# Kernel optimization log

Measured on AMD Instinct MI355X. Metric: run time of the kernel, lower is better.

## Reference

```python
import jax, jax.numpy as jnp
import numpy as np

EPS = 1e-5


def setup_inputs() -> dict:
    key = jax.random.key(0)
    ks = jax.random.split(key, 5)
    N, E, D, L = 10000, 160000, 512, 3
    x = jax.random.normal(ks[0], (N, D), dtype=jnp.float32)
    src = jax.random.randint(ks[1], (E,), 0, N, dtype=jnp.int64)
    dst = jax.random.randint(ks[2], (E,), 0, N, dtype=jnp.int64)
    gamma = jnp.ones((L, D), dtype=jnp.float32)
    beta = jnp.zeros((L, D), dtype=jnp.float32)
    # glorot-ish scale so ReLU stack stays well-conditioned
    W = jax.random.normal(ks[3], (L, D, D), dtype=jnp.float32) * (1.0 / np.sqrt(D))
    b = jnp.zeros((L, D), dtype=jnp.float32)
    return {"x": x, "src": src, "dst": dst, "gamma": gamma, "beta": beta, "W": W, "b": b}


def reference(x, src, dst, gamma, beta, W, b):
    N = x.shape[0]
    ones = jnp.ones(src.shape[0], dtype=x.dtype)
    # DGL GraphConv norm='both': src side uses out-degree, dst side uses in-degree
    out_deg = jnp.clip(jax.ops.segment_sum(ones, src, num_segments=N), 1.0)
    in_deg = jnp.clip(jax.ops.segment_sum(ones, dst, num_segments=N), 1.0)
    src_norm = (out_deg ** -0.5)[:, None]  # [N,1]
    dst_norm = (in_deg ** -0.5)[:, None]   # [N,1]
    n_layers = gamma.shape[0]
    for i in range(n_layers):
        # BatchNorm1d (training mode: batch mean, biased variance)
        mu = jnp.mean(x, axis=0)
        var = jnp.var(x, axis=0)
        x = (x - mu) * jax.lax.rsqrt(var + EPS) * gamma[i] + beta[i]
        h = x * src_norm
        agg = jax.ops.segment_sum(h[src], dst, num_segments=N) * dst_norm
        x = jax.nn.relu(agg @ W[i] + b[i])
    return x
```

## Files before the change

### kernel.cpp

```cpp
#include <hip/hip_runtime.h>
#include <hip/hip_bf16.h>

constexpr int N = 10000;
constexpr int D = 512;
constexpr int E = 160000;
constexpr int L = 3;
constexpr float EPS = 1e-5f;

constexpr int NSHARD = 8;
constexpr int SHCOL = D / NSHARD;

typedef _Float16 half8 __attribute__((ext_vector_type(8)));
typedef _Float16 half2v __attribute__((ext_vector_type(2)));
typedef float floatx4 __attribute__((ext_vector_type(4)));

__device__ __forceinline__ void glds16(const _Float16* g, _Float16* l) {
    __builtin_amdgcn_global_load_lds(
        (const __attribute__((address_space(1))) uint32_t*)(g),
        (__attribute__((address_space(3))) uint32_t*)(l),
        16, 0, 0);
}

constexpr int DEG_BLOCKS  = (E + 255) / 256;
constexpr int CONV_BLOCKS = 100;
constexpr int TW_BLOCKS   = L * 256;
constexpr int MEGA_BLOCKS = DEG_BLOCKS + CONV_BLOCKS + TW_BLOCKS;

__global__ __launch_bounds__(256) void mega_setup(
    const int* __restrict__ src, const int* __restrict__ dst,
    const float* __restrict__ x, const float* __restrict__ W,
    int* __restrict__ out_deg, int* __restrict__ in_deg,
    _Float16* __restrict__ x16, float* __restrict__ stats0,
    _Float16* __restrict__ Wt) {
    __shared__ float tb[32][33];
    int bid = blockIdx.x;
    int tid = threadIdx.x;
    if (bid < DEG_BLOCKS) {
        int e = bid * 256 + tid;
        if (e < E) {
            atomicAdd(&out_deg[src[e]], 1);
            atomicAdd(&in_deg[dst[e]], 1);
        }
    } else if (bid < DEG_BLOCKS + CONV_BLOCKS) {
        int b = bid - DEG_BLOCKS;
        int r0 = b * 100;
        int r1 = r0 + 100; if (r1 > N) r1 = N;
        int c2 = tid * 2;
        float s0 = 0.f, s1 = 0.f, q0 = 0.f, q1 = 0.f;
        for (int r = r0; r < r1; ++r) {
            float2 v = *(const float2*)(x + (size_t)r * D + c2);
            s0 += v.x; q0 += v.x * v.x;
            s1 += v.y; q1 += v.y * v.y;
            half2v h; h[0] = (_Float16)v.x; h[1] = (_Float16)v.y;
            *(half2v*)(x16 + (size_t)r * D + c2) = h;
        }
        atomicAdd(&stats0[c2], s0);
        atomicAdd(&stats0[c2 + 1], s1);
        atomicAdd(&stats0[D + c2], q0);
        atomicAdd(&stats0[D + c2 + 1], q1);
    } else {
        int b = bid - DEG_BLOCKS - CONV_BLOCKS;
        int l = b >> 8;
        int t = b & 255;
        int k0 = (t >> 4) * 32, n0 = (t & 15) * 32;
        int tx = tid & 31, ty = tid >> 5;
        const float* Wl = W + (size_t)l * D * D;
        _Float16* Wtl = Wt + (size_t)l * D * D;
        for (int i = 0; i < 32; i += 8)
            tb[ty + i][tx] = Wl[(size_t)(k0 + ty + i) * D + n0 + tx];
        __syncthreads();
        for (int i = 0; i < 32; i += 8)
            Wtl[(size_t)(n0 + ty + i) * D + k0 + tx] = (_Float16)tb[tx][ty + i];
    }
}

__global__ void scan_indeg(const int* __restrict__ in_deg,
                           const int* __restrict__ out_deg,
                           int* __restrict__ off, int* __restrict__ cursor,
                           float* __restrict__ src_norm, float* __restrict__ dst_norm) {
    __shared__ int lsum[1024];
    int t = threadIdx.x;
    const int chunk = (N + 1023) / 1024;
    int start = t * chunk;
    int end = start + chunk; if (end > N) end = N;
    int s = 0;
    for (int i = start; i < end; ++i) s += in_deg[i];
    lsum[t] = s;
    __syncthreads();
    for (int d = 1; d < 1024; d <<= 1) {
        int v = (t >= d) ? lsum[t - d] : 0;
        __syncthreads();
        lsum[t] += v;
        __syncthreads();
    }
    int excl = (t == 0) ? 0 : lsum[t - 1];
    for (int i = start; i < end; ++i) {
        off[i] = excl;
        cursor[i] = excl;
        excl += in_deg[i];
        int od = out_deg[i]; if (od < 1) od = 1;
        int id = in_deg[i];  if (id < 1) id = 1;
        src_norm[i] = rsqrtf((float)od);
        dst_norm[i] = rsqrtf((float)id);
    }
    if (t == 1023) off[N] = lsum[1023];
}

__global__ void csr_fill(const int* __restrict__ src, const int* __restrict__ dst,
                         int* __restrict__ cursor, int* __restrict__ csr_src) {
    int e = blockIdx.x * blockDim.x + threadIdx.x;
    if (e >= E) return;
    int d = dst[e];
    int pos = atomicAdd(&cursor[d], 1);
    csr_src[pos] = src[e];
}

__global__ __launch_bounds__(256) void aggregate_bn_shard(
    const _Float16* __restrict__ x, const int* __restrict__ off,
    const int* __restrict__ csr_src, const float* __restrict__ src_norm,
    const float* __restrict__ dst_norm, const float* __restrict__ stats,
    const float* __restrict__ gamma, const float* __restrict__ beta,
    _Float16* __restrict__ agg) {
    int shard = blockIdx.x & 7;
    int blk   = blockIdx.x >> 3;
    int wave  = threadIdx.x >> 6;
    int wid   = blk * 4 + wave;
    int lane  = threadIdx.x & 63;
    int half  = lane >> 5;
    int cl    = lane & 31;
    int c0    = shard * SHCOL + cl * 2;

    const float invN = 1.0f / (float)N;
    float2 sv = *(const float2*)(stats + c0);
    float2 qv = *(const float2*)(stats + D + c0);
    float2 gm = *(const float2*)(gamma + c0);
    float2 bt = *(const float2*)(beta + c0);
    float mu0 = sv.x * invN, mu1 = sv.y * invN;
    float var0 = qv.x * invN - mu0 * mu0;
    float var1 = qv.y * invN - mu1 * mu1;
    float sc0 = gm.x * rsqrtf(var0 + EPS);
    float sc1 = gm.y * rsqrtf(var1 + EPS);
    float sh0 = bt.x - mu0 * sc0;
    float sh1 = bt.y - mu1 * sc1;

    int e0 = off[wid], e1 = off[wid + 1];
    const _Float16* xs = x + c0;
    float a0 = 0.f, a1 = 0.f, b0 = 0.f, b1 = 0.f, tA = 0.f, tB = 0.f;
    int e = e0 + half;
    for (; e + 2 < e1; e += 4) {
        int sA = csr_src[e];
        int sB = csr_src[e + 2];
        float nA = src_norm[sA];
        float nB = src_norm[sB];
        half2v vA = *(const half2v*)(xs + (size_t)sA * D);
        half2v vB = *(const half2v*)(xs + (size_t)sB * D);
        a0 += (float)vA[0] * nA; a1 += (float)vA[1] * nA; tA += nA;
        b0 += (float)vB[0] * nB; b1 += (float)vB[1] * nB; tB += nB;
    }
    for (; e < e1; e += 2) {
        int sA = csr_src[e];
        float nA = src_norm[sA];
        half2v vA = *(const half2v*)(xs + (size_t)sA * D);
        a0 += (float)vA[0] * nA; a1 += (float)vA[1] * nA; tA += nA;
    }
    a0 += b0; a1 += b1;
    float t = tA + tB;
    a0 += __shfl_xor(a0, 32);
    a1 += __shfl_xor(a1, 32);
    t  += __shfl_xor(t, 32);
    if (half == 0) {
        float dn = dst_norm[wid];
        half2v o;
        o[0] = (_Float16)(dn * (sc0 * a0 + sh0 * t));
        o[1] = (_Float16)(dn * (sc1 * a1 + sh1 * t));
        *(half2v*)(agg + (size_t)wid * D + c0) = o;
    }
}

template <typename OutT, bool STATS>
__global__ __launch_bounds__(128) void mm_f16_relu(
    const _Float16* __restrict__ A, const _Float16* __restrict__ Bt,
    const float* __restrict__ bias, OutT* __restrict__ C, int M,
    float* __restrict__ stats) {
    __shared__ __align__(16) _Float16 As[2][64 * 64];
    __shared__ __align__(16) _Float16 Bs[2][128 * 64];
    const int tid  = threadIdx.x;
    const int wave = tid >> 6;
    const int lane = tid & 63;
    const int quad = lane >> 4;
    const int l16  = lane & 15;
    const int row0 = blockIdx.x * 64;
    const int col0 = blockIdx.y * 128;
    const int wn   = wave * 64;

    const int srl = lane >> 3;
    const int sq  = lane & 7;
    const int sqs = (sq ^ srl) * 8;

    const _Float16* gA[4];
    const _Float16* gB[8];
#pragma unroll
    for (int j = 0; j < 4; ++j) {
        int ar = row0 + wave * 32 + j * 8 + srl;
        if (ar >= M) ar = M - 1;
        gA[j] = A + (size_t)ar * D + sqs;
    }
#pragma unroll
    for (int j = 0; j < 8; ++j) {
        int br = col0 + wave * 64 + j * 8 + srl;
        gB[j] = Bt + (size_t)br * D + sqs;
    }

    const int l7 = l16 & 7;
    const int swz0 = (quad ^ l7) * 8;
    const int swz1 = ((4 + quad) ^ l7) * 8;

    floatx4 acc[4][4] = {};

    auto stage = [&](int buf, int k0) {
        _Float16* as = As[buf] + (wave * 32) * 64;
        _Float16* bs = Bs[buf] + (wave * 64) * 64;
#pragma unroll
        for (int j = 0; j < 4; ++j)
            glds16(gA[j] + k0, as + j * 8 * 64);
#pragma unroll
        for (int j = 0; j < 8; ++j)
            glds16(gB[j] + k0, bs + j * 8 * 64);
    };

    stage(0, 0);
    __syncthreads();

    int cur = 0;
    for (int kt = 0; kt < 8; ++kt) {
        if (kt < 7) stage(cur ^ 1, (kt + 1) * 64);
        const _Float16* asb = As[cur];
        const _Float16* bsb = Bs[cur];
        half8 af0[4], af1[4], bf0[4], bf1[4];
#pragma unroll
        for (int i = 0; i < 4; ++i) {
            int r = i * 16 + l16;
            af0[i] = *(const half8*)(asb + r * 64 + swz0);
            af1[i] = *(const half8*)(asb + r * 64 + swz1);
        }
#pragma unroll
        for (int j = 0; j < 4; ++j) {
            int r = wn + j * 16 + l16;
            bf0[j] = *(const half8*)(bsb + r * 64 + swz0);
            bf1[j] = *(const half8*)(bsb + r * 64 + swz1);
        }
#pragma unroll
        for (int i = 0; i < 4; ++i)
#pragma unroll
            for (int j = 0; j < 4; ++j)
                acc[i][j] = __builtin_amdgcn_mfma_f32_16x16x32_f16(
                    af0[i], bf0[j], acc[i][j], 0, 0, 0);
#pragma unroll
        for (int i = 0; i < 4; ++i)
#pragma unroll
            for (int j = 0; j < 4; ++j)
                acc[i][j] = __builtin_amdgcn_mfma_f32_16x16x32_f16(
                    af1[i], bf1[j], acc[i][j], 0, 0, 0);
        __syncthreads();
        cur ^= 1;
    }

    float s[4] = {}, q[4] = {};
#pragma unroll
    for (int i = 0; i < 4; ++i) {
#pragma unroll
        for (int r = 0; r < 4; ++r) {
            int row = row0 + i * 16 + quad * 4 + r;
            bool valid = row < M;
#pragma unroll
            for (int j = 0; j < 4; ++j) {
                int col = col0 + wn + j * 16 + l16;
                float v = acc[i][j][r] + bias[col];
                v = v > 0.f ? v : 0.f;
                if (valid) {
                    C[(size_t)row * D + col] = (OutT)v;
                    if (STATS) { s[j] += v; q[j] += v * v; }
                }
            }
        }
    }
    if (STATS) {
#pragma unroll
        for (int j = 0; j < 4; ++j) {
            float sv = s[j], qv = q[j];
            sv += __shfl_xor(sv, 16); sv += __shfl_xor(sv, 32);
            qv += __shfl_xor(qv, 16); qv += __shfl_xor(qv, 32);
            if (quad == 0) {
                int col = col0 + wn + j * 16 + l16;
                atomicAdd(&stats[col], sv);
                atomicAdd(&stats[D + col], qv);
            }
        }
    }
}

extern "C" void kernel_launch(void* const* d_in, const int* in_sizes, int n_in,
                              void* d_out, int out_size, void* d_ws, size_t ws_size,
                              hipStream_t stream) {
    const float* x_in  = (const float*)d_in[0];
    const int*   src   = (const int*)d_in[1];
    const int*   dst   = (const int*)d_in[2];
    const float* gamma = (const float*)d_in[3];
    const float* beta  = (const float*)d_in[4];
    const float* W     = (const float*)d_in[5];
    const float* b     = (const float*)d_in[6];
    float* out = (float*)d_out;

    char* p = (char*)d_ws;
    _Float16* x16 = (_Float16*)p;  p += (size_t)N * D * 2;
    _Float16* agg = (_Float16*)p;  p += (size_t)N * D * 2;
    _Float16* Wt  = (_Float16*)p;  p += (size_t)L * D * D * 2;
    float* src_norm = (float*)p;   p += (size_t)N * 4;
    float* dst_norm = (float*)p;   p += (size_t)N * 4;
    int* out_deg   = (int*)p;      p += (size_t)N * 4;
    int* in_deg    = (int*)p;      p += (size_t)N * 4;
    float* stats0  = (float*)p;    p += 2 * D * 4;
    float* stats1  = (float*)p;    p += 2 * D * 4;
    float* stats2  = (float*)p;    p += 2 * D * 4;
    int* csr_off   = (int*)p;      p += (size_t)(N + 1) * 4;
    int* cursor    = (int*)p;      p += (size_t)N * 4;
    int* csr_src   = (int*)p;      p += (size_t)E * 4;

    float* stats_in[3] = {stats0, stats1, stats2};

    hipMemsetAsync(out_deg, 0, (2 * (size_t)N + 6 * D) * sizeof(int), stream);
    mega_setup<<<MEGA_BLOCKS, 256, 0, stream>>>(src, dst, x_in, W,
                                                out_deg, in_deg, x16, stats0, Wt);
    scan_indeg<<<1, 1024, 0, stream>>>(in_deg, out_deg, csr_off, cursor,
                                       src_norm, dst_norm);
    csr_fill<<<DEG_BLOCKS, 256, 0, stream>>>(src, dst, cursor, csr_src);

    dim3 mm_grid((N + 63) / 64, D / 128);
    const int agg_blocks = NSHARD * ((N + 3) / 4);

    for (int l = 0; l < L; ++l) {
        const float* gl  = gamma + (size_t)l * D;
        const float* bl  = beta + (size_t)l * D;
        const _Float16* Wl = Wt + (size_t)l * D * D;
        const float* bil = b + (size_t)l * D;

        aggregate_bn_shard<<<agg_blocks, 256, 0, stream>>>(
            x16, csr_off, csr_src, src_norm, dst_norm, stats_in[l], gl, bl, agg);
        if (l == L - 1) {
            mm_f16_relu<float, false><<<mm_grid, 128, 0, stream>>>(
                agg, Wl, bil, out, N, nullptr);
        } else {
            mm_f16_relu<_Float16, true><<<mm_grid, 128, 0, stream>>>(
                agg, Wl, bil, x16, N, stats_in[l + 1]);
        }
    }
}
```

Baseline: 346.0 us.

## Replace column-sharded aggregation with one wave per node using 16-byte loads

```diff
diff --git a/kernel.cpp b/kernel.cpp
--- a/kernel.cpp
+++ b/kernel.cpp
@@ -7,9 +7,6 @@
 constexpr int L = 3;
 constexpr float EPS = 1e-5f;
 
-constexpr int NSHARD = 8;
-constexpr int SHCOL = D / NSHARD;
-
 typedef _Float16 half8 __attribute__((ext_vector_type(8)));
 typedef _Float16 half2v __attribute__((ext_vector_type(2)));
 typedef float floatx4 __attribute__((ext_vector_type(4)));
@@ -22,7 +19,7 @@
 }
 
 constexpr int DEG_BLOCKS  = (E + 255) / 256;
-constexpr int CONV_BLOCKS = 100;
+constexpr int CONV_BLOCKS = 1000;
 constexpr int TW_BLOCKS   = L * 256;
 constexpr int MEGA_BLOCKS = DEG_BLOCKS + CONV_BLOCKS + TW_BLOCKS;
 
@@ -43,8 +40,8 @@
         }
     } else if (bid < DEG_BLOCKS + CONV_BLOCKS) {
         int b = bid - DEG_BLOCKS;
-        int r0 = b * 100;
-        int r1 = r0 + 100; if (r1 > N) r1 = N;
+        int r0 = b * 10;
+        int r1 = r0 + 10; if (r1 > N) r1 = N;
         int c2 = tid * 2;
         float s0 = 0.f, s1 = 0.f, q0 = 0.f, q1 = 0.f;
         for (int r = r0; r < r1; ++r) {
@@ -115,66 +112,65 @@
     csr_src[pos] = src[e];
 }
 
-__global__ __launch_bounds__(256) void aggregate_bn_shard(
+__global__ __launch_bounds__(256) void aggregate_bn(
     const _Float16* __restrict__ x, const int* __restrict__ off,
     const int* __restrict__ csr_src, const float* __restrict__ src_norm,
     const float* __restrict__ dst_norm, const float* __restrict__ stats,
     const float* __restrict__ gamma, const float* __restrict__ beta,
     _Float16* __restrict__ agg) {
-    int shard = blockIdx.x & 7;
-    int blk   = blockIdx.x >> 3;
-    int wave  = threadIdx.x >> 6;
-    int wid   = blk * 4 + wave;
-    int lane  = threadIdx.x & 63;
-    int half  = lane >> 5;
-    int cl    = lane & 31;
-    int c0    = shard * SHCOL + cl * 2;
-
+    int wid = (blockIdx.x * 256 + threadIdx.x) >> 6;
+    if (wid >= N) return;
+    int lane = threadIdx.x & 63;
+    int c0 = lane * 8;
+
+    float scale[8], shift[8];
     const float invN = 1.0f / (float)N;
-    float2 sv = *(const float2*)(stats + c0);
-    float2 qv = *(const float2*)(stats + D + c0);
-    float2 gm = *(const float2*)(gamma + c0);
-    float2 bt = *(const float2*)(beta + c0);
-    float mu0 = sv.x * invN, mu1 = sv.y * invN;
-    float var0 = qv.x * invN - mu0 * mu0;
-    float var1 = qv.y * invN - mu1 * mu1;
-    float sc0 = gm.x * rsqrtf(var0 + EPS);
-    float sc1 = gm.y * rsqrtf(var1 + EPS);
-    float sh0 = bt.x - mu0 * sc0;
-    float sh1 = bt.y - mu1 * sc1;
+    for (int i = 0; i < 8; ++i) {
+        int c = c0 + i;
+        float mu = stats[c] * invN;
+        float var = stats[D + c] * invN - mu * mu;
+        float sc = gamma[c] * rsqrtf(var + EPS);
+        scale[i] = sc;
+        shift[i] = beta[c] - mu * sc;
+    }
 
     int e0 = off[wid], e1 = off[wid + 1];
-    const _Float16* xs = x + c0;
-    float a0 = 0.f, a1 = 0.f, b0 = 0.f, b1 = 0.f, tA = 0.f, tB = 0.f;
-    int e = e0 + half;
-    for (; e + 2 < e1; e += 4) {
-        int sA = csr_src[e];
-        int sB = csr_src[e + 2];
-        float nA = src_norm[sA];
-        float nB = src_norm[sB];
-        half2v vA = *(const half2v*)(xs + (size_t)sA * D);
-        half2v vB = *(const half2v*)(xs + (size_t)sB * D);
-        a0 += (float)vA[0] * nA; a1 += (float)vA[1] * nA; tA += nA;
-        b0 += (float)vB[0] * nB; b1 += (float)vB[1] * nB; tB += nB;
-    }
-    for (; e < e1; e += 2) {
-        int sA = csr_src[e];
-        float nA = src_norm[sA];
-        half2v vA = *(const half2v*)(xs + (size_t)sA * D);
-        a0 += (float)vA[0] * nA; a1 += (float)vA[1] * nA; tA += nA;
-    }
-    a0 += b0; a1 += b1;
-    float t = tA + tB;
-    a0 += __shfl_xor(a0, 32);
-    a1 += __shfl_xor(a1, 32);
-    t  += __shfl_xor(t, 32);
-    if (half == 0) {
-        float dn = dst_norm[wid];
-        half2v o;
-        o[0] = (_Float16)(dn * (sc0 * a0 + sh0 * t));
-        o[1] = (_Float16)(dn * (sc1 * a1 + sh1 * t));
-        *(half2v*)(agg + (size_t)wid * D + c0) = o;
-    }
+    float a[8] = {}, a2[8] = {};
+    float t = 0.f;
+    int e = e0;
+    for (; e + 4 <= e1; e += 4) {
+        int s0 = csr_src[e];
+        int s1 = csr_src[e + 1];
+        int s2 = csr_src[e + 2];
+        int s3 = csr_src[e + 3];
+        float n0 = src_norm[s0];
+        float n1 = src_norm[s1];
+        float n2 = src_norm[s2];
+        float n3 = src_norm[s3];
+        half8 v0 = *(const half8*)(x + (size_t)s0 * D + c0);
+        half8 v1 = *(const half8*)(x + (size_t)s1 * D + c0);
+        half8 v2 = *(const half8*)(x + (size_t)s2 * D + c0);
+        half8 v3 = *(const half8*)(x + (size_t)s3 * D + c0);
+        t += (n0 + n1) + (n2 + n3);
+        for (int k = 0; k < 8; ++k) {
+            a[k]  += (float)v0[k] * n0;
+            a2[k] += (float)v1[k] * n1;
+            a[k]  += (float)v2[k] * n2;
+            a2[k] += (float)v3[k] * n3;
+        }
+    }
+    for (; e < e1; ++e) {
+        int s0 = csr_src[e];
+        float n0 = src_norm[s0];
+        half8 v0 = *(const half8*)(x + (size_t)s0 * D + c0);
+        t += n0;
+        for (int k = 0; k < 8; ++k) a[k] += (float)v0[k] * n0;
+    }
+    float dn = dst_norm[wid];
+    half8 o;
+    for (int i = 0; i < 8; ++i)
+        o[i] = (_Float16)(dn * (scale[i] * (a[i] + a2[i]) + shift[i] * t));
+    *(half8*)(agg + (size_t)wid * D + c0) = o;
 }
 
 template <typename OutT, bool STATS>
@@ -336,7 +332,7 @@
     csr_fill<<<DEG_BLOCKS, 256, 0, stream>>>(src, dst, cursor, csr_src);
 
     dim3 mm_grid((N + 63) / 64, D / 128);
-    const int agg_blocks = NSHARD * ((N + 3) / 4);
+    const int agg_blocks = (N + 3) / 4;
 
     for (int l = 0; l < L; ++l) {
         const float* gl  = gamma + (size_t)l * D;
@@ -344,7 +340,7 @@
         const _Float16* Wl = Wt + (size_t)l * D * D;
         const float* bil = b + (size_t)l * D;
 
-        aggregate_bn_shard<<<agg_blocks, 256, 0, stream>>>(
+        aggregate_bn<<<agg_blocks, 256, 0, stream>>>(
             x16, csr_off, csr_src, src_norm, dst_norm, stats_in[l], gl, bl, agg);
         if (l == L - 1) {
             mm_f16_relu<float, false><<<mm_grid, 128, 0, stream>>>(
```

After: 317.6 us. 8.2% less time.
